# Kernel tuning notes

Measured on AMD Instinct MI355X. Metric: run time of the kernel, lower is better.

## Reference

```python
import jax, jax.numpy as jnp
import numpy as np
from jax import lax

B, D, T = 8, 768, 1024
H = 8
DH = D // H  # 96
FF = 4 * D
NUM_BUCKETS = 320
HALF = NUM_BUCKETS // 2      # 160
SMALL = HALF // 2            # 80
MAX_DIST = 800
CONV_K = 31
ATTN_SCALE = 32.0


def setup_inputs() -> dict:
    key = jax.random.key(0)
    ks = jax.random.split(key, 32)
    n = lambda i, shape, s=0.02: jax.random.normal(ks[i], shape, dtype=jnp.float32) * s
    return {
        "x": jax.random.normal(ks[0], (B, D, T), dtype=jnp.float32),
        # ff1
        "w_ff1a": n(1, (D, FF)), "b_ff1a": jnp.zeros((FF,)),
        "w_ff1b": n(2, (FF, D)), "b_ff1b": jnp.zeros((D,)),
        # attention
        "w_qkv": n(3, (D, 3 * D)), "b_qkv": jnp.zeros((3 * D,)),
        "w_out": n(4, (D, D)), "b_out": jnp.zeros((D,)),
        # gated relative position bias
        "rel_embed": n(5, (NUM_BUCKETS, H), 1.0),
        "gate_u": n(6, (H, DH)), "gate_w": n(7, (H, DH)),
        "gate_scale": jnp.ones((H,)),
        # conv module
        "gn1_w": jnp.ones((D,)), "gn1_b": jnp.zeros((D,)),
        "pw1_w": n(8, (2 * D, D)), "pw1_b": jnp.zeros((2 * D,)),
        "dw_w": n(9, (D, CONV_K)), "dw_b": jnp.zeros((D,)),
        "gn2_w": jnp.ones((D,)), "gn2_b": jnp.zeros((D,)),
        "pw2_w": n(10, (D, D)), "pw2_b": jnp.zeros((D,)),
        # ff2
        "w_ff2a": n(11, (D, FF)), "b_ff2a": jnp.zeros((FF,)),
        "w_ff2b": n(12, (FF, D)), "b_ff2b": jnp.zeros((D,)),
    }


def _rel_buckets(seq_len):
    pos = jnp.arange(seq_len)
    rp = pos[None, :] - pos[:, None]              # [T, T]
    sign = (rp >= 0).astype(jnp.int32)
    ra = jnp.abs(rp)
    is_small = ra < SMALL
    rc = jnp.maximum(ra, 1)
    log_ratio = jnp.log(rc.astype(jnp.float32) / SMALL) / np.float32(np.log(MAX_DIST / SMALL))
    log_pos = SMALL + (log_ratio * (HALF - SMALL)).astype(jnp.int32)  # trunc toward zero like .long()
    log_pos = jnp.minimum(log_pos, HALF - 1)
    bucket = jnp.where(is_small, ra, log_pos) + sign * HALF
    return jnp.clip(bucket, 0, NUM_BUCKETS - 1)


def _groupnorm1(xc, w, b, eps=1e-5):
    # GroupNorm(1, C): normalize over (C, T) per sample; xc: [B, C, T]
    m = xc.mean(axis=(1, 2), keepdims=True)
    v = xc.var(axis=(1, 2), keepdims=True)
    return (xc - m) * lax.rsqrt(v + eps) * w[None, :, None] + b[None, :, None]


def reference(x, w_ff1a, b_ff1a, w_ff1b, b_ff1b, w_qkv, b_qkv, w_out, b_out,
              rel_embed, gate_u, gate_w, gate_scale,
              gn1_w, gn1_b, pw1_w, pw1_b, dw_w, dw_b, gn2_w, gn2_b, pw2_w, pw2_b,
              w_ff2a, b_ff2a, w_ff2b, b_ff2b):
    b_, d_, t_ = x.shape
    s = jnp.swapaxes(x, 1, 2)                          # [B, T, D]

    ff = lambda t, wa, ba, wb, bb: jax.nn.gelu(t @ wa + ba, approximate=False) @ wb + bb
    s = s + 0.5 * ff(s, w_ff1a, b_ff1a, w_ff1b, b_ff1b)

    qkv = (s @ w_qkv + b_qkv).reshape(b_, t_, 3, H, DH)
    q = jnp.swapaxes(qkv[:, :, 0], 1, 2)               # [B, H, T, DH]
    k = jnp.swapaxes(qkv[:, :, 1], 1, 2)
    v = jnp.swapaxes(qkv[:, :, 2], 1, 2)

    # WavLM-style rescaled scores
    scores = jnp.einsum('bhtd,bhsd->bhts', q / ATTN_SCALE, k)
    scores = (scores - scores.max(axis=-1, keepdims=True)) * ATTN_SCALE
    scores = scores / np.float32(np.sqrt(DH))

    # gated relative position bias
    buckets = _rel_buckets(t_)                          # [T, T]
    dtab = jnp.transpose(rel_embed[buckets], (2, 0, 1))[None]  # [1, H, T, T]
    g_u = jax.nn.sigmoid(jnp.einsum('bhtd,hd->bht', q, gate_u))[..., None]  # [B,H,T,1]
    g_r = jax.nn.sigmoid(jnp.einsum('bhtd,hd->bht', q, gate_w))[..., None]
    r_tilde = gate_scale[None, :, None, None] * g_r * dtab
    rel_bias = dtab + g_u * dtab + (1.0 - g_u) * r_tilde

    probs = jax.nn.softmax(scores + rel_bias, axis=-1)
    attn = jnp.einsum('bhts,bhsd->bhtd', probs, v)
    attn = jnp.swapaxes(attn, 1, 2).reshape(b_, t_, d_)
    s = s + attn @ w_out + b_out

    # conv module
    c = jnp.swapaxes(s, 1, 2)                           # [B, D, T]
    h = _groupnorm1(c, gn1_w, gn1_b)
    h = jnp.einsum('od,bdt->bot', pw1_w, h) + pw1_b[None, :, None]  # 1x1 conv -> [B, 2D, T]
    a, g = jnp.split(h, 2, axis=1)
    h = a * jax.nn.sigmoid(g)                           # GLU over channels
    h = lax.conv_general_dilated(h, dw_w[:, None, :], (1,), [(CONV_K // 2, CONV_K // 2)],
                                 feature_group_count=d_,
                                 dimension_numbers=('NCH', 'OIH', 'NCH')) + dw_b[None, :, None]
    h = jax.nn.silu(_groupnorm1(h, gn2_w, gn2_b))
    h = jnp.einsum('od,bdt->bot', pw2_w, h) + pw2_b[None, :, None]
    c = c + h

    ct = jnp.swapaxes(c, 1, 2)
    s = ct + 0.5 * ff(ct, w_ff2a, b_ff2a, w_ff2b, b_ff2b)
    return jnp.swapaxes(s, 1, 2)                        # [B, D, T]
```

## Files before the change

### kernel.cpp

```cpp
#include <hip/hip_runtime.h>
#include <hip/hip_bf16.h>
#include <cstdint>

typedef __attribute__((ext_vector_type(8))) __bf16 bf16x8;
typedef __attribute__((ext_vector_type(4))) float f32x4;
typedef unsigned short u16t;

constexpr int Bn = 8, Dn = 768, Tn = 1024, Hn = 8, DHn = 96, FFn = 3072;
constexpr int BT = Bn * Tn;
constexpr float INV_SQRT_DH = 0.10206207261596575f;

#define GLDS16(gp, lp) __builtin_amdgcn_global_load_lds( \
    (__attribute__((address_space(1))) unsigned int*)(uintptr_t)(gp), \
    (__attribute__((address_space(3))) unsigned int*)(uintptr_t)(lp), 16, 0, 0)

__global__ void k_wtrans(const float* __restrict__ src, __hip_bfloat16* __restrict__ dst,
                         int K, int N) {
  __shared__ float t[32][33];
  int kb = blockIdx.y * 32, nb = blockIdx.x * 32;
  int tx = threadIdx.x, ty = threadIdx.y;
  for (int i = ty; i < 32; i += 8)
    t[i][tx] = src[(size_t)(kb + i) * N + nb + tx];
  __syncthreads();
  for (int i = ty; i < 32; i += 8)
    dst[(size_t)(nb + i) * K + kb + tx] = __float2bfloat16(t[tx][i]);
}

__global__ void k_wconv(const float* __restrict__ src, __hip_bfloat16* __restrict__ dst, int n) {
  int i = blockIdx.x * 256 + threadIdx.x;
  if (i < n) dst[i] = __float2bfloat16(src[i]);
}

__global__ void k_wpw1(const float* __restrict__ src, __hip_bfloat16* __restrict__ dst) {
  int i = blockIdx.x * 256 + threadIdx.x;
  if (i >= 1536 * 768) return;
  int n = i / 768, k = i - n * 768;
  int on = (n >> 1) + (n & 1) * 768;
  dst[i] = __float2bfloat16(src[(size_t)on * 768 + k]);
}

__global__ void k_reltab(const float* __restrict__ rel_embed, float* __restrict__ rel_tab) {
  int dd = blockIdx.x * 256 + threadIdx.x;
  if (dd >= 2047) return;
  int d = dd - 1023;
  int sign = d >= 0 ? 1 : 0;
  int ra = d < 0 ? -d : d;
  int base;
  if (ra < 80) base = ra;
  else {
    float lr = logf((float)ra / 80.0f) / 2.3025851f;
    int lp = 80 + (int)(lr * 80.0f);
    base = lp < 159 ? lp : 159;
  }
  int bucket = base + sign * 160;
  if (bucket < 0) bucket = 0;
  if (bucket > 319) bucket = 319;
  for (int h = 0; h < 8; ++h)
    rel_tab[h * 2047 + dd] = rel_embed[bucket * 8 + h];
}

__global__ void k_tin(const float* __restrict__ x, float* __restrict__ s,
                      __hip_bfloat16* __restrict__ sb) {
  __shared__ float t[32][33];
  int b = blockIdx.z;
  int t0 = blockIdx.x * 32, d0 = blockIdx.y * 32;
  int tx = threadIdx.x, ty = threadIdx.y;
  for (int i = ty; i < 32; i += 8)
    t[i][tx] = x[((size_t)b * Dn + d0 + i) * Tn + t0 + tx];
  __syncthreads();
  for (int i = ty; i < 32; i += 8) {
    float v = t[tx][i];
    size_t o = (size_t)(b * Tn + t0 + i) * Dn + d0 + tx;
    s[o] = v;
    sb[o] = __float2bfloat16(v);
  }
}

__global__ void k_tout(const float* __restrict__ s, float* __restrict__ out) {
  __shared__ float t[32][33];
  int b = blockIdx.z;
  int t0 = blockIdx.x * 32, d0 = blockIdx.y * 32;
  int tx = threadIdx.x, ty = threadIdx.y;
  for (int i = ty; i < 32; i += 8)
    t[i][tx] = s[(size_t)(b * Tn + t0 + i) * Dn + d0 + tx];
  __syncthreads();
  for (int i = ty; i < 32; i += 8)
    out[((size_t)b * Dn + d0 + i) * Tn + t0 + tx] = t[tx][i];
}

__global__ void k_vtrans(const __hip_bfloat16* __restrict__ qkv,
                         __hip_bfloat16* __restrict__ VT) {
  __shared__ __hip_bfloat16 t[32][33];
  int bh = blockIdx.z;
  int b = bh >> 3, h = bh & 7;
  int t0 = blockIdx.x * 32, d0 = blockIdx.y * 32;
  int tx = threadIdx.x, ty = threadIdx.y;
  for (int i = ty; i < 32; i += 8)
    t[i][tx] = qkv[(size_t)(b * Tn + t0 + i) * 2304 + 1536 + h * 96 + d0 + tx];
  __syncthreads();
  for (int i = ty; i < 32; i += 8)
    VT[((size_t)bh * 96 + d0 + i) * Tn + t0 + tx] = t[tx][i];
}

enum { EPI_BIAS = 0, EPI_GELU = 1, EPI_HALF_RES = 2, EPI_RES = 3, EPI_GLU = 4 };

template <int BM, int BN, int EPI>
__global__ __launch_bounds__(256)
void k_gemm(const __hip_bfloat16* __restrict__ A, const __hip_bfloat16* __restrict__ Bt,
            const float* __restrict__ bias, const float* __restrict__ resid,
            float* __restrict__ outF, __hip_bfloat16* __restrict__ outB,
            int M, int N, int K) {
  constexpr int MI = BM / 32;
  constexpr int NI = BN / 32;
  __shared__ __align__(16) __hip_bfloat16 lA[2][BM * 32];
  __shared__ __align__(16) __hip_bfloat16 lB[2][BN * 32];
  const int tid = threadIdx.x;
  const int lane = tid & 63, wv = tid >> 6;
  const int g = lane >> 4, c15 = lane & 15;
  const int gx = gridDim.x;
  const int nwg = gx * gridDim.y;
  const int orig = blockIdx.y * gx + blockIdx.x;
  const int q = nwg >> 3, rr = nwg & 7;
  const int xcd = orig & 7, idx = orig >> 3;
  const int wg = (xcd < rr ? xcd * (q + 1) : rr * (q + 1) + (xcd - rr) * q) + idx;
  const int m0 = (wg / gx) * BM, n0 = (wg % gx) * BN;
  const int wm = (wv >> 1) * (BM / 2), wn = (wv & 1) * (BN / 2);

  const int srow = lane >> 2, scol = (lane & 3) * 8;

  f32x4 acc[MI][NI] = {};

  auto stage = [&](int buf, int kt) {
#pragma unroll
    for (int c = 0; c < BM / 64; ++c) {
      int cid = wv * (BM / 64) + c;
      GLDS16(A + (size_t)(m0 + cid * 16 + srow) * K + kt + scol, &lA[buf][cid * 512]);
    }
#pragma unroll
    for (int c = 0; c < BN / 64; ++c) {
      int cid = wv * (BN / 64) + c;
      GLDS16(Bt + (size_t)(n0 + cid * 16 + srow) * K + kt + scol, &lB[buf][cid * 512]);
    }
  };

  const int nt = K >> 5;
  stage(0, 0);
  __syncthreads();
  int cur = 0;
  for (int t = 0; t < nt; ++t) {
    if (t + 1 < nt) stage(cur ^ 1, (t + 1) * 32);
    bf16x8 af[MI], bfr[NI];
#pragma unroll
    for (int i = 0; i < MI; ++i)
      af[i] = *(const bf16x8*)&lA[cur][(wm + i * 16 + c15) * 32 + g * 8];
#pragma unroll
    for (int j = 0; j < NI; ++j)
      bfr[j] = *(const bf16x8*)&lB[cur][(wn + j * 16 + c15) * 32 + g * 8];
#pragma unroll
    for (int i = 0; i < MI; ++i)
#pragma unroll
      for (int j = 0; j < NI; ++j)
        acc[i][j] = __builtin_amdgcn_mfma_f32_16x16x32_bf16(af[i], bfr[j], acc[i][j], 0, 0, 0);
    __syncthreads();
    cur ^= 1;
  }

#pragma unroll
  for (int i = 0; i < MI; ++i) {
    int row0 = m0 + wm + i * 16 + g * 4;
#pragma unroll
    for (int j = 0; j < NI; ++j) {
      int col = n0 + wn + j * 16 + c15;
      int bcol = (EPI == EPI_GLU) ? ((col >> 1) + (col & 1) * 768) : col;
      float bb = bias[bcol];
#pragma unroll
      for (int r = 0; r < 4; ++r) {
        int row = row0 + r;
        float v = acc[i][j][r] + bb;
        if (EPI == EPI_GELU) v = 0.5f * v * (1.0f + erff(v * 0.70710678118f));
        else if (EPI == EPI_HALF_RES) v = resid[(size_t)row * N + col] + 0.5f * v;
        else if (EPI == EPI_RES) v = resid[(size_t)row * N + col] + v;
        if (EPI == EPI_GLU) {
          float partner = __shfl_xor(v, 1);
          if (!(c15 & 1))
            outF[(size_t)row * (N >> 1) + (col >> 1)] =
                v * (1.0f / (1.0f + __expf(-partner)));
        } else {
          size_t o = (size_t)row * N + col;
          if (outF) outF[o] = v;
          if (outB) outB[o] = __float2bfloat16(v);
        }
      }
    }
  }
}

__global__ __launch_bounds__(256)
void k_attn(const __hip_bfloat16* __restrict__ qkv, const __hip_bfloat16* __restrict__ VT,
            const float* __restrict__ rel_tab,
            const float* __restrict__ gate_u, const float* __restrict__ gate_w,
            const float* __restrict__ gate_scale, __hip_bfloat16* __restrict__ ao) {
  __shared__ __align__(16) char smem[48128];
  __hip_bfloat16* kT = (__hip_bfloat16*)smem;
  __hip_bfloat16* vT = (__hip_bfloat16*)(smem + 13312);
  __hip_bfloat16* qT = (__hip_bfloat16*)(smem + 30208);
  __hip_bfloat16* pT = (__hip_bfloat16*)(smem + 30208);
  float* relLocal = (float*)(smem + 43520);
  float* cRow = (float*)(smem + 47872);

  const int tid = threadIdx.x, lane = tid & 63, wv = tid >> 6;
  const int g = lane >> 4, c15 = lane & 15;
  const int orig = blockIdx.y * 16 + blockIdx.x;
  const int wg = (orig & 7) * 128 + (orig >> 3);
  const int qt = wg & 15;
  const int bh = wg >> 4;
  const int b = bh >> 3, h = bh & 7;
  const int t0 = qt * 64;

  for (int i = tid; i < 1087; i += 256)
    relLocal[i] = rel_tab[h * 2047 + i + 960 - t0];

  {
    int r = tid >> 2, q4 = tid & 3;
    const __hip_bfloat16* src = qkv + (size_t)(b * Tn + t0 + r) * 2304 + h * 96 + q4 * 24;
    uint4 v0 = *(const uint4*)(src);
    uint4 v1 = *(const uint4*)(src + 8);
    uint4 v2 = *(const uint4*)(src + 16);
    *(uint4*)&qT[r * 104 + q4 * 24] = v0;
    *(uint4*)&qT[r * 104 + q4 * 24 + 8] = v1;
    *(uint4*)&qT[r * 104 + q4 * 24 + 16] = v2;
  }
  __syncthreads();

  if (tid < 64) {
    float du = 0.f, dw = 0.f;
#pragma unroll
    for (int c = 0; c < 12; ++c) {
      bf16x8 qv = *(const bf16x8*)&qT[tid * 104 + c * 8];
#pragma unroll
      for (int e = 0; e < 8; ++e) {
        float f = (float)qv[e];
        du += f * gate_u[h * 96 + c * 8 + e];
        dw += f * gate_w[h * 96 + c * 8 + e];
      }
    }
    float gu = 1.0f / (1.0f + __expf(-du));
    float gr = 1.0f / (1.0f + __expf(-dw));
    cRow[tid] = 1.0f + gu + (1.0f - gu) * gate_scale[h] * gr;
  }

  bf16x8 aQ[3];
#pragma unroll
  for (int c = 0; c < 3; ++c)
    aQ[c] = *(const bf16x8*)&qT[(wv * 16 + c15) * 104 + c * 32 + g * 8];
  __syncthreads();

  float crw[4];
#pragma unroll
  for (int r = 0; r < 4; ++r) crw[r] = cRow[wv * 16 + g * 4 + r];

  float mrow[4], ssum[4];
#pragma unroll
  for (int r = 0; r < 4; ++r) { mrow[r] = -1e30f; ssum[r] = 0.0f; }
  f32x4 accO[6] = {};

  for (int kt = 0; kt < 16; ++kt) {
    {
      int r = tid >> 2, q4 = tid & 3;
      const __hip_bfloat16* ks =
          qkv + (size_t)(b * Tn + kt * 64 + r) * 2304 + 768 + h * 96 + q4 * 24;
      uint4 k0 = *(const uint4*)(ks);
      uint4 k1 = *(const uint4*)(ks + 8);
      uint4 k2 = *(const uint4*)(ks + 16);
      *(uint4*)&kT[r * 104 + q4 * 24] = k0;
      *(uint4*)&kT[r * 104 + q4 * 24 + 8] = k1;
      *(uint4*)&kT[r * 104 + q4 * 24 + 16] = k2;
    }
    {
#pragma unroll
      for (int i = 0; i < 3; ++i) {
        int cid = i * 256 + tid;
        int row = cid >> 3, ch = cid & 7;
        const __hip_bfloat16* vs = VT + ((size_t)bh * 96 + row) * Tn + kt * 64 + ch * 8;
        *(uint4*)&vT[row * 88 + ch * 8] = *(const uint4*)vs;
      }
    }
    __syncthreads();

    f32x4 accS[4];
#pragma unroll
    for (int j = 0; j < 4; ++j) {
      f32x4 s = {};
#pragma unroll
      for (int c = 0; c < 3; ++c) {
        bf16x8 bk = *(const bf16x8*)&kT[(j * 16 + c15) * 104 + c * 32 + g * 8];
        s = __builtin_amdgcn_mfma_f32_16x16x32_bf16(aQ[c], bk, s, 0, 0, 0);
      }
      accS[j] = s;
    }

    float sv[4][4];
    const int tq_off = wv * 16 + g * 4;
#pragma unroll
    for (int j = 0; j < 4; ++j) {
      int tk = kt * 64 + j * 16 + c15;
#pragma unroll
      for (int r = 0; r < 4; ++r)
        sv[j][r] = accS[j][r] * INV_SQRT_DH + crw[r] * relLocal[tk - (tq_off + r) + 63];
    }

#pragma unroll
    for (int r = 0; r < 4; ++r) {
      float m = fmaxf(fmaxf(sv[0][r], sv[1][r]), fmaxf(sv[2][r], sv[3][r]));
#pragma unroll
      for (int off = 1; off < 16; off <<= 1) m = fmaxf(m, __shfl_xor(m, off, 64));
      float newm = fmaxf(mrow[r], m);
      float scale = __expf(mrow[r] - newm);
      float psum = 0.0f;
#pragma unroll
      for (int j = 0; j < 4; ++j) {
        float p = __expf(sv[j][r] - newm);
        sv[j][r] = p;
        psum += p;
      }
#pragma unroll
      for (int off = 1; off < 16; off <<= 1) psum += __shfl_xor(psum, off, 64);
      ssum[r] = ssum[r] * scale + psum;
      mrow[r] = newm;
#pragma unroll
      for (int f = 0; f < 6; ++f) accO[f][r] *= scale;
    }

#pragma unroll
    for (int j = 0; j < 4; ++j)
#pragma unroll
      for (int r = 0; r < 4; ++r)
        pT[wv * 1408 + (g * 4 + r) * 88 + j * 16 + c15] = __float2bfloat16(sv[j][r]);

#pragma unroll
    for (int c = 0; c < 2; ++c) {
      bf16x8 ap = *(const bf16x8*)&pT[wv * 1408 + c15 * 88 + c * 32 + g * 8];
#pragma unroll
      for (int f = 0; f < 6; ++f) {
        bf16x8 bv = *(const bf16x8*)&vT[(f * 16 + c15) * 88 + c * 32 + g * 8];
        accO[f] = __builtin_amdgcn_mfma_f32_16x16x32_bf16(ap, bv, accO[f], 0, 0, 0);
      }
    }
    __syncthreads();
  }

  float inv[4];
#pragma unroll
  for (int r = 0; r < 4; ++r) inv[r] = 1.0f / ssum[r];
#pragma unroll
  for (int f = 0; f < 6; ++f)
#pragma unroll
    for (int r = 0; r < 4; ++r) {
      int trow = t0 + wv * 16 + g * 4 + r;
      ao[(size_t)(b * Tn + trow) * Dn + h * 96 + f * 16 + c15] =
          __float2bfloat16(accO[f][r] * inv[r]);
    }
}

__global__ __launch_bounds__(256)
void k_dwconv(const float* __restrict__ in, const float* __restrict__ w,
              const float* __restrict__ bias, float* __restrict__ out) {
  __shared__ float tile[94][64];
  __shared__ float wt[64][31];
  __shared__ float bt[64];
  int b = blockIdx.z, t0 = blockIdx.x * 64, d0 = blockIdx.y * 64;
  int tid = threadIdx.x;
  for (int e = tid; e < 94 * 64; e += 256) {
    int rr = e >> 6, dd = e & 63;
    int t = t0 - 15 + rr;
    tile[rr][dd] = (t >= 0 && t < Tn) ? in[(size_t)(b * Tn + t) * Dn + d0 + dd] : 0.0f;
  }
  for (int e = tid; e < 64 * 31; e += 256) {
    int dd = e / 31, k = e - dd * 31;
    wt[dd][k] = w[(d0 + dd) * 31 + k];
  }
  if (tid < 64) bt[tid] = bias[d0 + tid];
  __syncthreads();
  for (int o = tid; o < 64 * 64; o += 256) {
    int tt = o >> 6, dd = o & 63;
    float s = bt[dd];
#pragma unroll
    for (int k = 0; k < 31; ++k) s += tile[tt + k][dd] * wt[dd][k];
    out[(size_t)(b * Tn + t0 + tt) * Dn + d0 + dd] = s;
  }
}

__global__ void k_gn_part(const float* __restrict__ x, float* __restrict__ part) {
  int b = blockIdx.y, c = blockIdx.x, tid = threadIdx.x;
  const float4* p = (const float4*)(x + (size_t)b * (Dn * Tn) + c * 8192);
  float s = 0.f, q = 0.f;
  for (int i = tid; i < 2048; i += 256) {
    float4 v = p[i];
    s += v.x + v.y + v.z + v.w;
    q += v.x * v.x + v.y * v.y + v.z * v.z + v.w * v.w;
  }
  for (int off = 1; off < 64; off <<= 1) {
    s += __shfl_xor(s, off, 64);
    q += __shfl_xor(q, off, 64);
  }
  __shared__ float ls[4], lq[4];
  int lane = tid & 63, wv = tid >> 6;
  if (lane == 0) { ls[wv] = s; lq[wv] = q; }
  __syncthreads();
  if (tid == 0) {
    part[(b * 96 + c) * 2] = ls[0] + ls[1] + ls[2] + ls[3];
    part[(b * 96 + c) * 2 + 1] = lq[0] + lq[1] + lq[2] + lq[3];
  }
}

__global__ void k_gn_final(const float* __restrict__ part, float* __restrict__ stats) {
  int b = blockIdx.x, tid = threadIdx.x;
  float s = 0.f, q = 0.f;
  if (tid < 96) { s = part[(b * 96 + tid) * 2]; q = part[(b * 96 + tid) * 2 + 1]; }
  for (int off = 1; off < 64; off <<= 1) {
    s += __shfl_xor(s, off, 64);
    q += __shfl_xor(q, off, 64);
  }
  __shared__ float ls[2], lq[2];
  int lane = tid & 63, wv = tid >> 6;
  if (lane == 0) { ls[wv] = s; lq[wv] = q; }
  __syncthreads();
  if (tid == 0) {
    const float N = (float)(Dn * Tn);
    float mean = (ls[0] + ls[1]) / N;
    float var = (lq[0] + lq[1]) / N - mean * mean;
    stats[b * 2] = mean;
    stats[b * 2 + 1] = rsqrtf(var + 1e-5f);
  }
}

template <bool SILU>
__global__ void k_gn_apply(const float* __restrict__ x, const float* __restrict__ stats,
                           const float* __restrict__ w, const float* __restrict__ bb,
                           __hip_bfloat16* __restrict__ out) {
  int i = blockIdx.x * 256 + threadIdx.x;
  if (i >= BT * Dn) return;
  int row = i / Dn, d = i - row * Dn;
  int b = row >> 10;
  float v = (x[i] - stats[b * 2]) * stats[b * 2 + 1] * w[d] + bb[d];
  if (SILU) v = v / (1.0f + __expf(-v));
  out[i] = __float2bfloat16(v);
}

extern "C" void kernel_launch(void* const* d_in, const int* in_sizes, int n_in,
                              void* d_out, int out_size, void* d_ws, size_t ws_size,
                              hipStream_t stream) {
  const float* x         = (const float*)d_in[0];
  const float* w_ff1a    = (const float*)d_in[1];
  const float* b_ff1a    = (const float*)d_in[2];
  const float* w_ff1b    = (const float*)d_in[3];
  const float* b_ff1b    = (const float*)d_in[4];
  const float* w_qkv     = (const float*)d_in[5];
  const float* b_qkv     = (const float*)d_in[6];
  const float* w_out     = (const float*)d_in[7];
  const float* b_out     = (const float*)d_in[8];
  const float* rel_embed = (const float*)d_in[9];
  const float* gate_u    = (const float*)d_in[10];
  const float* gate_w    = (const float*)d_in[11];
  const float* gate_sc   = (const float*)d_in[12];
  const float* gn1_w     = (const float*)d_in[13];
  const float* gn1_b     = (const float*)d_in[14];
  const float* pw1_w     = (const float*)d_in[15];
  const float* pw1_b     = (const float*)d_in[16];
  const float* dw_w      = (const float*)d_in[17];
  const float* dw_b      = (const float*)d_in[18];
  const float* gn2_w     = (const float*)d_in[19];
  const float* gn2_b     = (const float*)d_in[20];
  const float* pw2_w     = (const float*)d_in[21];
  const float* pw2_b     = (const float*)d_in[22];
  const float* w_ff2a    = (const float*)d_in[23];
  const float* b_ff2a    = (const float*)d_in[24];
  const float* w_ff2b    = (const float*)d_in[25];
  const float* b_ff2b    = (const float*)d_in[26];

  char* ws = (char*)d_ws;
  size_t off = 0;
  auto alloc = [&](size_t bytes) {
    void* p = ws + off;
    off = (off + bytes + 255) & ~(size_t)255;
    return p;
  };

  float* SA = (float*)alloc((size_t)BT * Dn * 4);
  float* SB = (float*)alloc((size_t)BT * Dn * 4);
  __hip_bfloat16* ABF = (__hip_bfloat16*)alloc((size_t)BT * Dn * 2);
  void* BIG = alloc((size_t)BT * FFn * 2);
  void* QKV = alloc((size_t)BT * 2304 * 2);
  __hip_bfloat16* Wf1a = (__hip_bfloat16*)alloc((size_t)Dn * FFn * 2);
  __hip_bfloat16* Wf1b = (__hip_bfloat16*)alloc((size_t)Dn * FFn * 2);
  __hip_bfloat16* Wqkv = (__hip_bfloat16*)alloc((size_t)Dn * 2304 * 2);
  __hip_bfloat16* Wout = (__hip_bfloat16*)alloc((size_t)Dn * Dn * 2);
  __hip_bfloat16* Wpw1 = (__hip_bfloat16*)alloc((size_t)1536 * Dn * 2);
  __hip_bfloat16* Wpw2 = (__hip_bfloat16*)alloc((size_t)Dn * Dn * 2);
  __hip_bfloat16* Wf2a = (__hip_bfloat16*)alloc((size_t)Dn * FFn * 2);
  __hip_bfloat16* Wf2b = (__hip_bfloat16*)alloc((size_t)Dn * FFn * 2);
  float* RELT  = (float*)alloc(8 * 2047 * 4);
  float* GPART = (float*)alloc(8 * 96 * 2 * 4);
  float* GSTAT = (float*)alloc(8 * 2 * 4);
  __hip_bfloat16* VT = (__hip_bfloat16*)BIG;
  float* GLUF = (float*)QKV;
  float* DWO = (float*)d_out;

  dim3 blk32(32, 8);
  k_wtrans<<<dim3(FFn / 32, Dn / 32), blk32, 0, stream>>>(w_ff1a, Wf1a, Dn, FFn);
  k_wtrans<<<dim3(Dn / 32, FFn / 32), blk32, 0, stream>>>(w_ff1b, Wf1b, FFn, Dn);
  k_wtrans<<<dim3(2304 / 32, Dn / 32), blk32, 0, stream>>>(w_qkv, Wqkv, Dn, 2304);
  k_wtrans<<<dim3(Dn / 32, Dn / 32), blk32, 0, stream>>>(w_out, Wout, Dn, Dn);
  k_wpw1<<<(1536 * Dn + 255) / 256, 256, 0, stream>>>(pw1_w, Wpw1);
  k_wconv<<<(Dn * Dn + 255) / 256, 256, 0, stream>>>(pw2_w, Wpw2, Dn * Dn);
  k_wtrans<<<dim3(FFn / 32, Dn / 32), blk32, 0, stream>>>(w_ff2a, Wf2a, Dn, FFn);
  k_wtrans<<<dim3(Dn / 32, FFn / 32), blk32, 0, stream>>>(w_ff2b, Wf2b, FFn, Dn);
  k_reltab<<<8, 256, 0, stream>>>(rel_embed, RELT);

  k_tin<<<dim3(Tn / 32, Dn / 32, Bn), blk32, 0, stream>>>(x, SA, ABF);

  k_gemm<128, 128, EPI_GELU><<<dim3(FFn / 128, BT / 128), 256, 0, stream>>>(
      ABF, Wf1a, b_ff1a, nullptr, nullptr, (__hip_bfloat16*)BIG, BT, FFn, Dn);
  k_gemm<64, 128, EPI_HALF_RES><<<dim3(Dn / 128, BT / 64), 256, 0, stream>>>(
      (__hip_bfloat16*)BIG, Wf1b, b_ff1b, SA, SB, ABF, BT, Dn, FFn);

  k_gemm<128, 128, EPI_BIAS><<<dim3(2304 / 128, BT / 128), 256, 0, stream>>>(
      ABF, Wqkv, b_qkv, nullptr, nullptr, (__hip_bfloat16*)QKV, BT, 2304, Dn);

  k_vtrans<<<dim3(Tn / 32, 3, 64), blk32, 0, stream>>>((const __hip_bfloat16*)QKV, VT);

  k_attn<<<dim3(16, 64), 256, 0, stream>>>((const __hip_bfloat16*)QKV, VT, RELT,
                                           gate_u, gate_w, gate_sc, ABF);

  k_gemm<64, 128, EPI_RES><<<dim3(Dn / 128, BT / 64), 256, 0, stream>>>(
      ABF, Wout, b_out, SB, SA, nullptr, BT, Dn, Dn);

  k_gn_part<<<dim3(96, 8), 256, 0, stream>>>(SA, GPART);
  k_gn_final<<<8, 128, 0, stream>>>(GPART, GSTAT);
  k_gn_apply<false><<<(BT * Dn + 255) / 256, 256, 0, stream>>>(SA, GSTAT, gn1_w, gn1_b, ABF);

  k_gemm<64, 128, EPI_GLU><<<dim3(1536 / 128, BT / 64), 256, 0, stream>>>(
      ABF, Wpw1, pw1_b, nullptr, GLUF, nullptr, BT, 1536, Dn);
  k_dwconv<<<dim3(Tn / 64, Dn / 64, Bn), 256, 0, stream>>>(GLUF, dw_w, dw_b, DWO);
  k_gn_part<<<dim3(96, 8), 256, 0, stream>>>(DWO, GPART);
  k_gn_final<<<8, 128, 0, stream>>>(GPART, GSTAT);
  k_gn_apply<true><<<(BT * Dn + 255) / 256, 256, 0, stream>>>(DWO, GSTAT, gn2_w, gn2_b, ABF);

  k_gemm<64, 128, EPI_RES><<<dim3(Dn / 128, BT / 64), 256, 0, stream>>>(
      ABF, Wpw2, pw2_b, SA, SB, ABF, BT, Dn, Dn);

  k_gemm<128, 128, EPI_GELU><<<dim3(FFn / 128, BT / 128), 256, 0, stream>>>(
      ABF, Wf2a, b_ff2a, nullptr, nullptr, (__hip_bfloat16*)BIG, BT, FFn, Dn);
  k_gemm<64, 128, EPI_HALF_RES><<<dim3(Dn / 128, BT / 64), 256, 0, stream>>>(
      (__hip_bfloat16*)BIG, Wf2b, b_ff2b, SB, SA, nullptr, BT, Dn, FFn);

  k_tout<<<dim3(Tn / 32, Dn / 32, Bn), blk32, 0, stream>>>(SA, (float*)d_out);
}
```

Measured before the change: 652.7 us.

## Fuse weight prep kernels, read V from global, add lazy softmax rescale in attention

After: 659.7 us. About the same (+1.1%).

```diff
diff --git a/kernel.cpp b/kernel.cpp
--- a/kernel.cpp
+++ b/kernel.cpp
@@ -14,49 +14,76 @@
     (__attribute__((address_space(1))) unsigned int*)(uintptr_t)(gp), \
     (__attribute__((address_space(3))) unsigned int*)(uintptr_t)(lp), 16, 0, 0)
 
-__global__ void k_wtrans(const float* __restrict__ src, __hip_bfloat16* __restrict__ dst,
-                         int K, int N) {
+__global__ void k_prep(const float* __restrict__ w_ff1a, const float* __restrict__ w_ff1b,
+                       const float* __restrict__ w_qkv, const float* __restrict__ w_out,
+                       const float* __restrict__ w_ff2a, const float* __restrict__ w_ff2b,
+                       const float* __restrict__ pw1_w, const float* __restrict__ pw2_w,
+                       const float* __restrict__ rel_embed,
+                       __hip_bfloat16* __restrict__ Wf1a, __hip_bfloat16* __restrict__ Wf1b,
+                       __hip_bfloat16* __restrict__ Wqkv, __hip_bfloat16* __restrict__ Wout,
+                       __hip_bfloat16* __restrict__ Wf2a, __hip_bfloat16* __restrict__ Wf2b,
+                       __hip_bfloat16* __restrict__ Wpw1, __hip_bfloat16* __restrict__ Wpw2,
+                       float* __restrict__ rel_tab) {
   __shared__ float t[32][33];
-  int kb = blockIdx.y * 32, nb = blockIdx.x * 32;
-  int tx = threadIdx.x, ty = threadIdx.y;
-  for (int i = ty; i < 32; i += 8)
-    t[i][tx] = src[(size_t)(kb + i) * N + nb + tx];
-  __syncthreads();
-  for (int i = ty; i < 32; i += 8)
-    dst[(size_t)(nb + i) * K + kb + tx] = __float2bfloat16(t[tx][i]);
-}
-
-__global__ void k_wconv(const float* __restrict__ src, __hip_bfloat16* __restrict__ dst, int n) {
-  int i = blockIdx.x * 256 + threadIdx.x;
-  if (i < n) dst[i] = __float2bfloat16(src[i]);
-}
-
-__global__ void k_wpw1(const float* __restrict__ src, __hip_bfloat16* __restrict__ dst) {
-  int i = blockIdx.x * 256 + threadIdx.x;
-  if (i >= 1536 * 768) return;
-  int n = i / 768, k = i - n * 768;
-  int on = (n >> 1) + (n & 1) * 768;
-  dst[i] = __float2bfloat16(src[(size_t)on * 768 + k]);
-}
-
-__global__ void k_reltab(const float* __restrict__ rel_embed, float* __restrict__ rel_tab) {
-  int dd = blockIdx.x * 256 + threadIdx.x;
-  if (dd >= 2047) return;
-  int d = dd - 1023;
-  int sign = d >= 0 ? 1 : 0;
-  int ra = d < 0 ? -d : d;
-  int base;
-  if (ra < 80) base = ra;
+  const int tid = threadIdx.x;
+  int bid = blockIdx.x;
+
+  const float* tsrc = nullptr;
+  __hip_bfloat16* tdst = nullptr;
+  int K = 0, N = 0;
+  if (bid < 2304) { tsrc = w_ff1a; tdst = Wf1a; K = 768; N = 3072; }
+  else if ((bid -= 2304) < 2304) { tsrc = w_ff1b; tdst = Wf1b; K = 3072; N = 768; }
+  else if ((bid -= 2304) < 1728) { tsrc = w_qkv; tdst = Wqkv; K = 768; N = 2304; }
+  else if ((bid -= 1728) < 576)  { tsrc = w_out; tdst = Wout; K = 768; N = 768; }
+  else if ((bid -= 576) < 2304)  { tsrc = w_ff2a; tdst = Wf2a; K = 768; N = 3072; }
+  else if ((bid -= 2304) < 2304) { tsrc = w_ff2b; tdst = Wf2b; K = 3072; N = 768; }
   else {
-    float lr = logf((float)ra / 80.0f) / 2.3025851f;
-    int lp = 80 + (int)(lr * 80.0f);
-    base = lp < 159 ? lp : 159;
-  }
-  int bucket = base + sign * 160;
-  if (bucket < 0) bucket = 0;
-  if (bucket > 319) bucket = 319;
-  for (int h = 0; h < 8; ++h)
-    rel_tab[h * 2047 + dd] = rel_embed[bucket * 8 + h];
+    bid -= 2304;
+    if (bid < 1152) {
+      int i4 = bid * 1024 + tid * 4;
+      int n = i4 / 768, k = i4 - n * 768;
+      int on = (n >> 1) + (n & 1) * 768;
+      float4 v = *(const float4*)(pw1_w + (size_t)on * 768 + k);
+      __hip_bfloat16* d = Wpw1 + i4;
+      d[0] = __float2bfloat16(v.x); d[1] = __float2bfloat16(v.y);
+      d[2] = __float2bfloat16(v.z); d[3] = __float2bfloat16(v.w);
+    } else if ((bid -= 1152) < 576) {
+      int i4 = bid * 1024 + tid * 4;
+      float4 v = *(const float4*)(pw2_w + i4);
+      __hip_bfloat16* d = Wpw2 + i4;
+      d[0] = __float2bfloat16(v.x); d[1] = __float2bfloat16(v.y);
+      d[2] = __float2bfloat16(v.z); d[3] = __float2bfloat16(v.w);
+    } else {
+      bid -= 576;
+      int dd = bid * 256 + tid;
+      if (dd < 2047) {
+        int d = dd - 1023;
+        int sign = d >= 0 ? 1 : 0;
+        int ra = d < 0 ? -d : d;
+        int base;
+        if (ra < 80) base = ra;
+        else {
+          float lr = logf((float)ra / 80.0f) / 2.3025851f;
+          int lp = 80 + (int)(lr * 80.0f);
+          base = lp < 159 ? lp : 159;
+        }
+        int bucket = base + sign * 160;
+        if (bucket < 0) bucket = 0;
+        if (bucket > 319) bucket = 319;
+        for (int h = 0; h < 8; ++h)
+          rel_tab[h * 2047 + dd] = rel_embed[bucket * 8 + h];
+      }
+    }
+    return;
+  }
+  int nb32 = N / 32;
+  int nb = (bid % nb32) * 32, kb = (bid / nb32) * 32;
+  int tx = tid & 31, ty = tid >> 5;
+  for (int i = ty; i < 32; i += 8)
+    t[i][tx] = tsrc[(size_t)(kb + i) * N + nb + tx];
+  __syncthreads();
+  for (int i = ty; i < 32; i += 8)
+    tdst[(size_t)(nb + i) * K + kb + tx] = __float2bfloat16(t[tx][i]);
 }
 
 __global__ void k_tin(const float* __restrict__ x, float* __restrict__ s,
@@ -195,18 +222,17 @@
   }
 }
 
-__global__ __launch_bounds__(256)
+__global__ __launch_bounds__(256, 4)
 void k_attn(const __hip_bfloat16* __restrict__ qkv, const __hip_bfloat16* __restrict__ VT,
             const float* __restrict__ rel_tab,
             const float* __restrict__ gate_u, const float* __restrict__ gate_w,
             const float* __restrict__ gate_scale, __hip_bfloat16* __restrict__ ao) {
-  __shared__ __align__(16) char smem[48128];
+  __shared__ __align__(16) char smem[31232];
   __hip_bfloat16* kT = (__hip_bfloat16*)smem;
-  __hip_bfloat16* vT = (__hip_bfloat16*)(smem + 13312);
-  __hip_bfloat16* qT = (__hip_bfloat16*)(smem + 30208);
-  __hip_bfloat16* pT = (__hip_bfloat16*)(smem + 30208);
-  float* relLocal = (float*)(smem + 43520);
-  float* cRow = (float*)(smem + 47872);
+  __hip_bfloat16* qT = (__hip_bfloat16*)(smem + 13312);
+  __hip_bfloat16* pT = (__hip_bfloat16*)(smem + 13312);
+  float* relLocal = (float*)(smem + 26624);
+  float* cRow = (float*)(smem + 30976);
 
   const int tid = threadIdx.x, lane = tid & 63, wv = tid >> 6;
   const int g = lane >> 4, c15 = lane & 15;
@@ -264,7 +290,10 @@
   for (int r = 0; r < 4; ++r) { mrow[r] = -1e30f; ssum[r] = 0.0f; }
   f32x4 accO[6] = {};
 
+  const __hip_bfloat16* vbase = VT + ((size_t)bh * 96 + c15) * Tn + g * 8;
+
   for (int kt = 0; kt < 16; ++kt) {
+    __syncthreads();
     {
       int r = tid >> 2, q4 = tid & 3;
       const __hip_bfloat16* ks =
@@ -276,15 +305,6 @@
       *(uint4*)&kT[r * 104 + q4 * 24 + 8] = k1;
       *(uint4*)&kT[r * 104 + q4 * 24 + 16] = k2;
     }
-    {
-#pragma unroll
-      for (int i = 0; i < 3; ++i) {
-        int cid = i * 256 + tid;
-        int row = cid >> 3, ch = cid & 7;
-        const __hip_bfloat16* vs = VT + ((size_t)bh * 96 + row) * Tn + kt * 64 + ch * 8;
-        *(uint4*)&vT[row * 88 + ch * 8] = *(const uint4*)vs;
-      }
-    }
     __syncthreads();
 
     f32x4 accS[4];
@@ -309,26 +329,39 @@
         sv[j][r] = accS[j][r] * INV_SQRT_DH + crw[r] * relLocal[tk - (tq_off + r) + 63];
     }
 
+    float pmax[4];
 #pragma unroll
     for (int r = 0; r < 4; ++r) {
       float m = fmaxf(fmaxf(sv[0][r], sv[1][r]), fmaxf(sv[2][r], sv[3][r]));
 #pragma unroll
       for (int off = 1; off < 16; off <<= 1) m = fmaxf(m, __shfl_xor(m, off, 64));
-      float newm = fmaxf(mrow[r], m);
-      float scale = __expf(mrow[r] - newm);
-      float psum = 0.0f;
+      pmax[r] = m;
+    }
+    int grow = (pmax[0] > mrow[0] + 8.0f) | (pmax[1] > mrow[1] + 8.0f) |
+               (pmax[2] > mrow[2] + 8.0f) | (pmax[3] > mrow[3] + 8.0f);
+    if (__any(grow)) {
+#pragma unroll
+      for (int r = 0; r < 4; ++r) {
+        float newm = fmaxf(mrow[r], pmax[r]);
+        float sc = __expf(mrow[r] - newm);
+        ssum[r] *= sc;
+        mrow[r] = newm;
+#pragma unroll
+        for (int f = 0; f < 6; ++f) accO[f][r] *= sc;
+      }
+    }
+#pragma unroll
+    for (int r = 0; r < 4; ++r) {
+      float ps = 0.0f;
 #pragma unroll
       for (int j = 0; j < 4; ++j) {
-        float p = __expf(sv[j][r] - newm);
+        float p = __expf(sv[j][r] - mrow[r]);
         sv[j][r] = p;
-        psum += p;
+        ps += p;
       }
 #pragma unroll
-      for (int off = 1; off < 16; off <<= 1) psum += __shfl_xor(psum, off, 64);
-      ssum[r] = ssum[r] * scale + psum;
-      mrow[r] = newm;
-#pragma unroll
-      for (int f = 0; f < 6; ++f) accO[f][r] *= scale;
+      for (int off = 1; off < 16; off <<= 1) ps += __shfl_xor(ps, off, 64);
+      ssum[r] += ps;
     }
 
 #pragma unroll
@@ -337,16 +370,16 @@
       for (int r = 0; r < 4; ++r)
         pT[wv * 1408 + (g * 4 + r) * 88 + j * 16 + c15] = __float2bfloat16(sv[j][r]);
 
-#pragma unroll
-    for (int c = 0; c < 2; ++c) {
-      bf16x8 ap = *(const bf16x8*)&pT[wv * 1408 + c15 * 88 + c * 32 + g * 8];
-#pragma unroll
-      for (int f = 0; f < 6; ++f) {
-        bf16x8 bv = *(const bf16x8*)&vT[(f * 16 + c15) * 88 + c * 32 + g * 8];
-        accO[f] = __builtin_amdgcn_mfma_f32_16x16x32_bf16(ap, bv, accO[f], 0, 0, 0);
-      }
-    }
-    __syncthreads();
+    bf16x8 ap0 = *(const bf16x8*)&pT[wv * 1408 + c15 * 88 + g * 8];
+    bf16x8 ap1 = *(const bf16x8*)&pT[wv * 1408 + c15 * 88 + 32 + g * 8];
+    const __hip_bfloat16* vrow = vbase + kt * 64;
+#pragma unroll
+    for (int f = 0; f < 6; ++f) {
+      bf16x8 bv0 = *(const bf16x8*)(vrow + (size_t)f * 16 * Tn);
+      bf16x8 bv1 = *(const bf16x8*)(vrow + (size_t)f * 16 * Tn + 32);
+      accO[f] = __builtin_amdgcn_mfma_f32_16x16x32_bf16(ap0, bv0, accO[f], 0, 0, 0);
+      accO[f] = __builtin_amdgcn_mfma_f32_16x16x32_bf16(ap1, bv1, accO[f], 0, 0, 0);
+    }
   }
 
   float inv[4];
@@ -507,15 +540,11 @@
   float* DWO = (float*)d_out;
 
   dim3 blk32(32, 8);
-  k_wtrans<<<dim3(FFn / 32, Dn / 32), blk32, 0, stream>>>(w_ff1a, Wf1a, Dn, FFn);
-  k_wtrans<<<dim3(Dn / 32, FFn / 32), blk32, 0, stream>>>(w_ff1b, Wf1b, FFn, Dn);
-  k_wtrans<<<dim3(2304 / 32, Dn / 32), blk32, 0, stream>>>(w_qkv, Wqkv, Dn, 2304);
-  k_wtrans<<<dim3(Dn / 32, Dn / 32), blk32, 0, stream>>>(w_out, Wout, Dn, Dn);
-  k_wpw1<<<(1536 * Dn + 255) / 256, 256, 0, stream>>>(pw1_w, Wpw1);
-  k_wconv<<<(Dn * Dn + 255) / 256, 256, 0, stream>>>(pw2_w, Wpw2, Dn * Dn);
-  k_wtrans<<<dim3(FFn / 32, Dn / 32), blk32, 0, stream>>>(w_ff2a, Wf2a, Dn, FFn);
-  k_wtrans<<<dim3(Dn / 32, FFn / 32), blk32, 0, stream>>>(w_ff2b, Wf2b, FFn, Dn);
-  k_reltab<<<8, 256, 0, stream>>>(rel_embed, RELT);
+
+  const int PREP_BLOCKS = 2304 + 2304 + 1728 + 576 + 2304 + 2304 + 1152 + 576 + 8;
+  k_prep<<<PREP_BLOCKS, 256, 0, stream>>>(
+      w_ff1a, w_ff1b, w_qkv, w_out, w_ff2a, w_ff2b, pw1_w, pw2_w, rel_embed,
+      Wf1a, Wf1b, Wqkv, Wout, Wf2a, Wf2b, Wpw1, Wpw2, RELT);
 
   k_tin<<<dim3(Tn / 32, Dn / 32, Bn), blk32, 0, stream>>>(x, SA, ABF);
 
```
